# Performance work log

Measured on AMD Instinct MI355X. Metric: run time of the kernel, lower is better.

## Reference

```python
import jax, jax.numpy as jnp
import numpy as np

N_WIRES = 14
N_LAYERS = 3
DIM = 2 ** N_WIRES
BATCH = 1024


def _rx(theta):
    # RX(t) = [[cos t/2, -i sin t/2], [-i sin t/2, cos t/2]]
    c = jnp.cos(theta / 2).astype(jnp.complex64)
    s = jnp.sin(theta / 2).astype(jnp.complex64)
    return jnp.stack([jnp.stack([c, -1j * s]), jnp.stack([-1j * s, c])])


def _ry(theta):
    # RY(t) = [[cos t/2, -sin t/2], [sin t/2, cos t/2]]
    c = jnp.cos(theta / 2).astype(jnp.complex64)
    s = jnp.sin(theta / 2).astype(jnp.complex64)
    return jnp.stack([jnp.stack([c, -s]), jnp.stack([s, c])])


def _apply_1q(psi, U, w):
    # psi: (B, 2, 2, ..., 2); apply 2x2 U on qubit axis w+1
    psi = jnp.tensordot(psi, U, axes=((w + 1,), (1,)))  # contracted axis moves to end
    return jnp.moveaxis(psi, -1, w + 1)


def _apply_cnot(psi, c, t):
    # control qubit c, target qubit t (Python ints)
    a0 = jax.lax.index_in_dim(psi, 0, axis=c + 1, keepdims=True)
    a1 = jax.lax.index_in_dim(psi, 1, axis=c + 1, keepdims=True)
    a1 = jnp.flip(a1, axis=t + 1)  # X on target within control=1 subspace
    return jnp.concatenate([a0, a1], axis=c + 1)


def _circuit_features(state, params):
    # state: (B, 2**n) real normalized amplitudes -> PauliZ expvals (B, n)
    n = N_WIRES
    psi = state.astype(jnp.complex64).reshape((-1,) + (2,) * n)
    for layer in range(N_LAYERS):
        for w in range(n):
            psi = _apply_1q(psi, _rx(params[layer, w, 0]), w)
            psi = _apply_1q(psi, _ry(params[layer, w, 1]), w)
        for w in range(n - 1):
            psi = _apply_cnot(psi, w, w + 1)
        psi = _apply_cnot(psi, n - 1, 0)
    probs = jnp.real(psi * jnp.conj(psi))  # (B, 2, ..., 2)
    feats = []
    for w in range(n):
        axes = tuple(a for a in range(1, n + 1) if a != w + 1)
        p = jnp.sum(probs, axis=axes)  # (B, 2)
        feats.append(p[:, 0] - p[:, 1])  # <Z_w>
    return jnp.stack(feats, axis=1)  # (B, n)


def setup_inputs() -> dict:
    key = jax.random.key(0)
    k1, k2, k3 = jax.random.split(key, 3)
    state = jax.random.normal(k1, (BATCH, DIM), dtype=jnp.float32)
    state = state / jnp.linalg.norm(state, axis=1, keepdims=True)  # valid statevectors
    params = jax.random.normal(k2, (N_LAYERS, N_WIRES, 2), dtype=jnp.float32)
    head_w = jax.random.normal(k3, (1, N_WIRES), dtype=jnp.float32) * (1.0 / np.sqrt(N_WIRES))
    head_b = jnp.zeros((1,), dtype=jnp.float32)
    return {"state": state, "params": params, "head_w": head_w, "head_b": head_b}


def reference(state, params, head_w, head_b):
    feats = _circuit_features(state, params)          # (B, n_wires)
    out = feats @ head_w.T + head_b                   # (B, 1)
    return out[:, 0]                                  # (B,)
```

## Files before the change

### kernel.cpp

```cpp
#include <hip/hip_runtime.h>
#include <utility>

#define NW 14
#define NL 3
#define DIM 16384
#define NG  (NL * NW)
#define TPB 1024
#define NPH3 11

typedef float v2f __attribute__((ext_vector_type(2)));

struct S3 {
    int ok = 1;
    unsigned Lane[NPH3][6] = {};
    unsigned Reg[NPH3][4]  = {};
    unsigned Vw[4]         = {};
    unsigned WT[NPH3][6]   = {};
    unsigned WS[NPH3][16]  = {};
    unsigned pv[NPH3][4]   = {};
    unsigned cp[NPH3][4]   = {};
    unsigned ST[10] = {}, STK[4] = {}, STJ[4] = {};
    unsigned pz[NW] = {}, nib[NW] = {};
};

constexpr int rank14(const unsigned* v, int n) {
    unsigned piv[14] = {};
    int r = 0;
    for (int i = 0; i < n; ++i) {
        unsigned x = v[i];
        for (int bit = 13; bit >= 0; --bit) {
            if (!((x >> bit) & 1u)) continue;
            if (piv[bit]) { x ^= piv[bit]; }
            else { piv[bit] = x; ++r; x = 0; break; }
        }
    }
    return r;
}

constexpr unsigned coords14(const unsigned bas[14], unsigned v, int& ok) {
    unsigned pv14[14] = {}, pc14[14] = {};
    for (int b = 0; b < 14; ++b) {
        unsigned x = bas[b], c = 1u << b;
        for (int bit = 13; bit >= 0; --bit) {
            if (!((x >> bit) & 1u)) continue;
            if (pv14[bit]) { x ^= pv14[bit]; c ^= pc14[bit]; }
            else { pv14[bit] = x; pc14[bit] = c; x = 0; break; }
        }
        if (x) ok = 0;
    }
    unsigned x = v, c = 0;
    for (int bit = 13; bit >= 0; --bit) {
        if ((x >> bit) & 1u) {
            if (!pv14[bit]) { ok = 0; return 0; }
            x ^= pv14[bit]; c ^= pc14[bit];
        }
    }
    return c;
}

constexpr S3 build3() {
    S3 S{};
    unsigned mk[NG] = {}, vmg[NG] = {}, zm[NW] = {};
    {
        unsigned A[NW] = {};
        for (int w = 0; w < NW; ++w) A[w] = 1u << (NW - 1 - w);
        int g = 0;
        for (int l = 0; l < NL; ++l) {
            unsigned rows[NW] = {};
            for (int u = 0; u < NW; ++u) rows[u] = A[u] | (1u << (NW + u));
            for (int col = 0; col < NW; ++col) {
                int piv = col;
                while (piv < NW && !((rows[piv] >> col) & 1u)) ++piv;
                if (piv >= NW) { S.ok = 0; continue; }
                unsigned tmp = rows[col]; rows[col] = rows[piv]; rows[piv] = tmp;
                for (int r = 0; r < NW; ++r)
                    if (r != col && ((rows[r] >> col) & 1u)) rows[r] ^= rows[col];
            }
            for (int w = 0; w < NW; ++w) {
                unsigned m = 0;
                for (int r = 0; r < NW; ++r) m |= ((rows[r] >> (NW + w)) & 1u) << r;
                mk[g] = m; vmg[g] = A[w]; ++g;
            }
            for (int w = 0; w < NW - 1; ++w) A[w + 1] ^= A[w];
            A[0] ^= A[NW - 1];
        }
        for (int w = 0; w < NW; ++w) zm[w] = A[w];
    }
    for (int p = 0; p < NPH3; ++p) {
        int J = (p < 10) ? 4 : 2;
        for (int q = 0; q < J; ++q) S.Reg[p][q] = mk[4 * p + q];
    }
    {
        int found = 0;
        for (unsigned seed = 1; seed < 256u && !found; ++seed) {
            unsigned cand[4] = {};
            for (int i = 0; i < 4; ++i) {
                unsigned h = (seed * 2654435761u) ^ ((unsigned)(i + 1) * 0x9E3779B9u);
                h ^= h >> 15; h *= 2246822519u; h ^= h >> 13; h *= 3266489917u; h ^= h >> 16;
                cand[i] = h & 0x3FFFu;
            }
            if (rank14(cand, 4) != 4) continue;
            int good = 1;
            for (int g = 0; g < 6 && good; ++g) {
                int nm = (g < 5) ? 8 : 2;
                unsigned set[12] = {}; int n = 0;
                for (int i = 0; i < nm; ++i) set[n++] = mk[8 * g + i];
                for (int i = 0; i < 4; ++i) set[n++] = cand[i];
                if (rank14(set, n) != n) good = 0;
            }
            if (good) { for (int i = 0; i < 4; ++i) S.Vw[i] = cand[i]; found = 1; }
        }
        if (!found) S.ok = 0;
    }
    for (int g = 0; g < 6; ++g) {
        int nm = (g < 5) ? 8 : 2;
        unsigned bas[14] = {}; int nb = 0;
        for (int i = 0; i < 4; ++i) bas[nb++] = S.Vw[i];
        for (int i = 0; i < nm; ++i) bas[nb++] = mk[8 * g + i];
        unsigned fill[12] = {}; int nf = 0;
        for (int b = 0; b < 14 && nb < 14; ++b) {
            unsigned t[15] = {};
            for (int i = 0; i < nb; ++i) t[i] = bas[i];
            t[nb] = 1u << b;
            if (rank14(t, nb + 1) == nb + 1) { bas[nb++] = 1u << b; fill[nf++] = 1u << b; }
        }
        if (nb != 14) S.ok = 0;
        if (g < 5) {
            int pA = 2 * g, pB = 2 * g + 1;
            for (int b = 0; b < 4; ++b) { S.Lane[pA][b] = S.Reg[pB][b]; S.Lane[pB][b] = S.Reg[pA][b]; }
            S.Lane[pA][4] = fill[0]; S.Lane[pA][5] = fill[1];
            S.Lane[pB][4] = fill[0]; S.Lane[pB][5] = fill[1];
        } else {
            S.Reg[10][2] = fill[0]; S.Reg[10][3] = fill[1];
            for (int b = 0; b < 6; ++b) S.Lane[10][b] = fill[2 + b];
        }
    }
    for (int t = NPH3 - 2; t >= 0; --t) {
        unsigned bas[14] = {};
        for (int b = 0; b < 6; ++b) bas[b] = S.Lane[t + 1][b];
        for (int q = 0; q < 4; ++q) bas[6 + q] = S.Reg[t + 1][q];
        for (int j = 0; j < 4; ++j) bas[10 + j] = S.Vw[j];
        unsigned rb[4] = {}; int rn = 0;
        for (int b = 0; b < 6; ++b) {
            int bestcs = 0, bestg = -1; unsigned bestr = 0;
            for (int cs = 0; cs < 16; ++cs) {
                unsigned c = 0;
                for (int q = 0; q < 4; ++q) if ((cs >> q) & 1) c ^= S.Reg[t][q];
                int ok2 = 1;
                unsigned r = coords14(bas, S.Lane[t][b] ^ c, ok2) & 15u;
                if (!ok2) continue;
                unsigned x = r;
                for (int i = 0; i < rn; ++i) {
                    int hb = 3; while (hb > 0 && !((rb[i] >> hb) & 1u)) --hb;
                    if ((x >> hb) & 1u) x ^= rb[i];
                }
                int gain = x ? 1 : 0;
                if (gain > bestg) { bestg = gain; bestcs = cs; bestr = r; }
                if (gain == 1) break;
            }
            unsigned c = 0;
            for (int q = 0; q < 4; ++q) if ((bestcs >> q) & 1) c ^= S.Reg[t][q];
            S.Lane[t][b] ^= c;
            unsigned x = bestr;
            for (int i = 0; i < rn; ++i) {
                int hb = 3; while (hb > 0 && !((rb[i] >> hb) & 1u)) --hb;
                if ((x >> hb) & 1u) x ^= rb[i];
            }
            if (x && rn < 4) rb[rn++] = x;
        }
        int okc = 1;
        for (int b = 0; b < 6; ++b) S.WT[t][b] = coords14(bas, S.Lane[t][b], okc);
        for (int s = 0; s < 16; ++s) {
            unsigned v = 0;
            for (int q = 0; q < 4; ++q) if ((s >> q) & 1) v ^= S.Reg[t][q];
            S.WS[t][s] = coords14(bas, v, okc);
        }
        if (!okc) S.ok = 0;
        if ((t & 1) == 0) {
            for (int b = 0; b < 6; ++b) if (S.WT[t][b] >> 10) S.ok = 0;
            for (int s = 0; s < 16; ++s) if (S.WS[t][s] >> 10) S.ok = 0;
        }
        for (int ub = 0; ub < 10; ++ub) {
            unsigned wamp = (ub < 6) ? S.Lane[t][ub] : S.Vw[ub - 6];
            unsigned widx = (ub < 6) ? S.WT[t][ub] : (1u << (10 + ub - 6));
            unsigned ramp = 0;
            for (int b = 0; b < 6; ++b) if ((widx >> b) & 1u) ramp ^= S.Lane[t + 1][b];
            for (int q = 0; q < 4; ++q) if ((widx >> (6 + q)) & 1u) ramp ^= S.Reg[t + 1][q];
            for (int j = 0; j < 4; ++j) if ((widx >> (10 + j)) & 1u) ramp ^= S.Vw[j];
            if (ramp != wamp) S.ok = 0;
        }
        for (int q = 0; q < 4; ++q) {
            unsigned widx = S.WS[t][1u << q];
            unsigned ramp = 0;
            for (int b = 0; b < 6; ++b) if ((widx >> b) & 1u) ramp ^= S.Lane[t + 1][b];
            for (int qq = 0; qq < 4; ++qq) if ((widx >> (6 + qq)) & 1u) ramp ^= S.Reg[t + 1][qq];
            for (int j = 0; j < 4; ++j) if ((widx >> (10 + j)) & 1u) ramp ^= S.Vw[j];
            if (ramp != S.Reg[t][q]) S.ok = 0;
        }
    }
    for (int p = 0; p < NPH3; ++p) {
        int J = (p < 10) ? 4 : 2;
        for (int q = 0; q < J; ++q) {
            unsigned vm = vmg[4 * p + q], pvm = 0;
            for (int b = 0; b < 6; ++b)
                if (__builtin_popcount(S.Lane[p][b] & vm) & 1) pvm |= 1u << b;
            for (int j = 0; j < 4; ++j)
                if (__builtin_popcount(S.Vw[j] & vm) & 1) pvm |= 1u << (6 + j);
            S.pv[p][q] = pvm;
            unsigned cpm = 0;
            for (int s = 0; s < 16; ++s) {
                unsigned v = 0;
                for (int q2 = 0; q2 < 4; ++q2) if ((s >> q2) & 1) v ^= S.Reg[p][q2];
                if (__builtin_popcount(v & vm) & 1) cpm |= 1u << s;
            }
            S.cp[p][q] = cpm;
        }
    }
    {
        unsigned bas[14] = {};
        for (int b = 0; b < 6; ++b) bas[b] = S.Lane[0][b];
        for (int q = 0; q < 4; ++q) bas[6 + q] = S.Reg[0][q];
        for (int j = 0; j < 4; ++j) bas[10 + j] = S.Vw[j];
        int okc = 1;
        for (int b = 0; b < 10; ++b) S.ST[b] = coords14(bas, 1u << (b + 2), okc);
        for (int k = 0; k < 4; ++k) S.STK[k] = coords14(bas, (unsigned)k << 12, okc);
        for (int j = 0; j < 4; ++j) S.STJ[j] = coords14(bas, (unsigned)j, okc);
        if (!okc) S.ok = 0;
        for (int ub = 0; ub < 18; ++ub) {
            unsigned amp = (ub < 10) ? (1u << (ub + 2))
                         : (ub < 14) ? ((unsigned)(ub - 10) << 12) : (unsigned)(ub - 14);
            unsigned widx = (ub < 10) ? S.ST[ub] : (ub < 14) ? S.STK[ub - 10] : S.STJ[ub - 14];
            unsigned ramp = 0;
            for (int b = 0; b < 6; ++b) if ((widx >> b) & 1u) ramp ^= S.Lane[0][b];
            for (int q = 0; q < 4; ++q) if ((widx >> (6 + q)) & 1u) ramp ^= S.Reg[0][q];
            for (int j = 0; j < 4; ++j) if ((widx >> (10 + j)) & 1u) ramp ^= S.Vw[j];
            if (ramp != amp) S.ok = 0;
        }
    }
    for (int w = 0; w < NW; ++w) {
        unsigned pzm = 0;
        for (int b = 0; b < 6; ++b)
            if (__builtin_popcount(S.Lane[10][b] & zm[w]) & 1) pzm |= 1u << b;
        for (int j = 0; j < 4; ++j)
            if (__builtin_popcount(S.Vw[j] & zm[w]) & 1) pzm |= 1u << (6 + j);
        S.pz[w] = pzm;
        unsigned nv = 0;
        for (int q = 0; q < 4; ++q)
            if (__builtin_popcount(S.Reg[10][q] & zm[w]) & 1) nv |= 1u << q;
        S.nib[w] = nv;
    }
    return S;
}
constexpr S3 SC3 = build3();
static_assert(SC3.ok == 1, "schedule build failed");

template<class F, unsigned... I>
__device__ __forceinline__ void static_for_impl(F&& f, std::integer_sequence<unsigned, I...>) {
    (f(std::integral_constant<unsigned, I>{}), ...);
}
template<unsigned N, class F>
__device__ __forceinline__ void static_for(F&& f) {
    static_for_impl(static_cast<F&&>(f), std::make_integer_sequence<unsigned, N>{});
}

template<int NEGLO, int NEGHI>
__device__ __forceinline__ v2f cmul(v2f k, v2f x) {
    v2f y;
    if constexpr (!NEGLO)
        asm("v_pk_mul_f32 %0, %1, %2 op_sel:[0,0] op_sel_hi:[0,1]"
            : "=&v"(y) : "v"(k), "v"(x));
    else
        asm("v_pk_mul_f32 %0, %1, %2 op_sel:[0,0] op_sel_hi:[0,1] neg_lo:[1,0] neg_hi:[1,0]"
            : "=&v"(y) : "v"(k), "v"(x));
    if constexpr (!NEGHI)
        asm("v_pk_fma_f32 %0, %1, %2, %0 op_sel:[1,1,0] op_sel_hi:[1,0,1] neg_lo:[0,1,0]"
            : "+v"(y) : "v"(k), "v"(x));
    else
        asm("v_pk_fma_f32 %0, %1, %2, %0 op_sel:[1,1,0] op_sel_hi:[1,0,1] neg_lo:[1,1,0] neg_hi:[1,0,0]"
            : "+v"(y) : "v"(k), "v"(x));
    return y;
}
template<int NEGLO, int NEGHI>
__device__ __forceinline__ void cmac(v2f& y, v2f k, v2f x) {
    if constexpr (!NEGLO)
        asm("v_pk_fma_f32 %0, %1, %2, %0 op_sel:[0,0,0] op_sel_hi:[0,1,1]"
            : "+v"(y) : "v"(k), "v"(x));
    else
        asm("v_pk_fma_f32 %0, %1, %2, %0 op_sel:[0,0,0] op_sel_hi:[0,1,1] neg_lo:[1,0,0] neg_hi:[1,0,0]"
            : "+v"(y) : "v"(k), "v"(x));
    if constexpr (!NEGHI)
        asm("v_pk_fma_f32 %0, %1, %2, %0 op_sel:[1,1,0] op_sel_hi:[1,0,1] neg_lo:[0,1,0]"
            : "+v"(y) : "v"(k), "v"(x));
    else
        asm("v_pk_fma_f32 %0, %1, %2, %0 op_sel:[1,1,0] op_sel_hi:[1,0,1] neg_lo:[1,1,0] neg_hi:[1,0,0]"
            : "+v"(y) : "v"(k), "v"(x));
}
template<bool CS> __device__ __forceinline__ v2f  cmulA(v2f k, v2f x) { return cmul<0, CS ? 1 : 0>(k, x); }
template<bool CS> __device__ __forceinline__ void cmacB(v2f& y, v2f k, v2f x) { cmac<CS ? 1 : 0, 0>(y, k, x); }

__global__ __launch_bounds__(TPB) void qsim_kernel(
    const float* __restrict__ state,
    const float* __restrict__ params,
    const float* __restrict__ head_w,
    const float* __restrict__ head_b,
    float* __restrict__ out)
{
    __shared__ v2f    psi[DIM];
    __shared__ float4 umat[NG];
    __shared__ float  red[TPB / 64];
    char* psiB = (char*)psi;
    const unsigned tid = threadIdx.x;

    if (tid < NG) {
        float t1 = 0.5f * params[2 * tid + 0];
        float t2 = 0.5f * params[2 * tid + 1];
        float s1, c1, s2, c2;
        sincosf(t1, &s1, &c1);
        sincosf(t2, &s2, &c2);
        umat[tid] = make_float4(c1 * c2, s1 * s2, -s2 * c1, -c2 * s1);
    }

    unsigned sidx = 0;
    static_for<10>([&](auto Bc) {
        constexpr int b = (int)decltype(Bc)::value;
        sidx ^= SC3.ST[b] & (unsigned)(-(int)((tid >> b) & 1u));
    });
    const float4* st4 = reinterpret_cast<const float4*>(state) + (size_t)blockIdx.x * (DIM / 4);
    static_for<4>([&](auto Kc) {
        constexpr int k = (int)decltype(Kc)::value;
        float4 v = st4[tid + k * TPB];
        const unsigned bi = sidx ^ SC3.STK[k];
        *(v2f*)(psiB + ((bi ^ SC3.STJ[0]) << 3)) = (v2f){ v.x, 0.f };
        *(v2f*)(psiB + ((bi ^ SC3.STJ[1]) << 3)) = (v2f){ v.y, 0.f };
        *(v2f*)(psiB + ((bi ^ SC3.STJ[2]) << 3)) = (v2f){ v.z, 0.f };
        *(v2f*)(psiB + ((bi ^ SC3.STJ[3]) << 3)) = (v2f){ v.w, 0.f };
    });
    __syncthreads();

    const unsigned rbase = ((tid >> 6) << 13) | ((tid & 63u) << 3);
    v2f x[16];

    static_for<NPH3>([&](auto Pc) {
        constexpr int P = (int)decltype(Pc)::value;
        static_for<16>([&](auto Sc) {
            constexpr int s = (int)decltype(Sc)::value;
            x[s] = *(const v2f*)(psiB + rbase + (s << 9));
        });
        static_for<4>([&](auto Qc) {
            constexpr int q = (int)decltype(Qc)::value;
            if constexpr (q < ((P < 10) ? 4 : 2)) {
                constexpr unsigned cp  = SC3.cp[P][q];
                constexpr unsigned pvm = SC3.pv[P][q];
                const float4 u = umat[4 * P + q];
                const unsigned sm = ((unsigned)__popc(tid & pvm)) << 31;
                v2f A, B;
                A.x = u.x; A.y = __uint_as_float(__float_as_uint(u.y) ^ sm);
                B.x = __uint_as_float(__float_as_uint(u.z) ^ sm); B.y = u.w;
                static_for<8>([&](auto Pp) {
                    constexpr unsigned pp   = decltype(Pp)::value;
                    constexpr unsigned lowm = (1u << q) - 1u;
                    constexpr unsigned s0   = ((pp & ~lowm) << 1) | (pp & lowm);
                    constexpr unsigned s1   = s0 | (1u << q);
                    constexpr bool c0 = (cp >> s0) & 1u;
                    constexpr bool c1 = (cp >> s1) & 1u;
                    const v2f x0 = x[s0], x1 = x[s1];
                    v2f y0 = cmulA<c0>(A, x0); cmacB<c0>(y0, B, x1);
                    v2f y1 = cmulA<c1>(A, x1); cmacB<c1>(y1, B, x0);
                    x[s0] = y0; x[s1] = y1;
                });
            }
        });
        if constexpr (P < 10) {
            if constexpr (P & 1) __syncthreads();
            unsigned wi = (tid >> 6) << 10;
            static_for<6>([&](auto Bc) {
                constexpr int b = (int)decltype(Bc)::value;
                wi ^= SC3.WT[P][b] & (unsigned)(-(int)((tid >> b) & 1u));
            });
            static_for<16>([&](auto Sc) {
                constexpr int s = (int)decltype(Sc)::value;
                *(v2f*)(psiB + ((wi ^ SC3.WS[P][s]) << 3)) = x[s];
            });
            if constexpr (P & 1) __syncthreads();
        }
    });

    float e[NW];
    static_for<NW>([&](auto Wc) {
        constexpr int w = (int)decltype(Wc)::value;
        constexpr unsigned pzw = SC3.pz[w];
        float hw = head_w[w];
        e[w] = (__popc(tid & pzw) & 1) ? -hw : hw;
    });
    float c[16];
    static_for<16>([&](auto Mc) { c[decltype(Mc)::value] = 0.f; });
    static_for<NW>([&](auto Wc) {
        constexpr int w = (int)decltype(Wc)::value;
        c[SC3.nib[w]] += e[w];
    });
    static_for<4>([&](auto Bc) {
        constexpr unsigned B = 1u << decltype(Bc)::value;
        static_for<16>([&](auto Kc) {
            constexpr unsigned k = decltype(Kc)::value;
            if constexpr (!(k & B)) {
                float a = c[k], b = c[k | B];
                c[k] = a + b; c[k | B] = a - b;
            }
        });
    });
    float acc = 0.f;
    static_for<16>([&](auto Sc) {
        constexpr int s = (int)decltype(Sc)::value;
        acc += (x[s].x * x[s].x + x[s].y * x[s].y) * c[s];
    });

#pragma unroll
    for (int off = 32; off > 0; off >>= 1)
        acc += __shfl_down(acc, off, 64);
    const unsigned lane = tid & 63, wv = tid >> 6;
    if (lane == 0) red[wv] = acc;
    __syncthreads();
    if (tid == 0) {
        float tot = 0.f;
#pragma unroll
        for (int i = 0; i < TPB / 64; ++i) tot += red[i];
        out[blockIdx.x] = tot + head_b[0];
    }
}

extern "C" void kernel_launch(void* const* d_in, const int* in_sizes, int n_in,
                              void* d_out, int out_size, void* d_ws, size_t ws_size,
                              hipStream_t stream) {
    const float* state  = (const float*)d_in[0];
    const float* params = (const float*)d_in[1];
    const float* head_w = (const float*)d_in[2];
    const float* head_b = (const float*)d_in[3];
    float* out = (float*)d_out;

    qsim_kernel<<<out_size, TPB, 0, stream>>>(state, params, head_w, head_b, out);
}
```

Baseline: 133.6 us.

## Halve LDS state buffer with two-pass bounce exchange to allow two blocks per CU

Replaces the full 128KB shared statevector with a half-size bounce buffer. Each exchange is split into two passes, with groups of threads writing or reading depending on a dropped index bit, and the schedule search is extended so that bit can be dropped consistently. Launch bounds now request higher occupancy so more than one block can be resident per CU. In exchange, every exchange needs twice as many barriers and extra registers to hold pending values, which may cut into the occupancy gain.

```diff
diff --git a/kernel.cpp b/kernel.cpp
--- a/kernel.cpp
+++ b/kernel.cpp
@@ -23,42 +23,43 @@
     unsigned pz[NW] = {}, nib[NW] = {};
 };
 
-constexpr int rank14(const unsigned* v, int n) {
-    unsigned piv[14] = {};
-    int r = 0;
-    for (int i = 0; i < n; ++i) {
-        unsigned x = v[i];
-        for (int bit = 13; bit >= 0; --bit) {
-            if (!((x >> bit) & 1u)) continue;
-            if (piv[bit]) { x ^= piv[bit]; }
-            else { piv[bit] = x; ++r; x = 0; break; }
-        }
-    }
-    return r;
-}
-
-constexpr unsigned coords14(const unsigned bas[14], unsigned v, int& ok) {
-    unsigned pv14[14] = {}, pc14[14] = {};
+struct Bas14 { unsigned piv[14] = {}; int n = 0; };
+constexpr bool binsert(Bas14& B, unsigned v) {
+    unsigned x = v;
+    for (int bit = 13; bit >= 0; --bit) {
+        if (!((x >> bit) & 1u)) continue;
+        if (B.piv[bit]) x ^= B.piv[bit];
+        else { B.piv[bit] = x; ++B.n; return true; }
+    }
+    return false;
+}
+
+struct Ech { unsigned pv14[14] = {}; unsigned pc14[14] = {}; int ok = 1; };
+constexpr Ech mkech(const unsigned bas[14]) {
+    Ech E{};
     for (int b = 0; b < 14; ++b) {
         unsigned x = bas[b], c = 1u << b;
         for (int bit = 13; bit >= 0; --bit) {
             if (!((x >> bit) & 1u)) continue;
-            if (pv14[bit]) { x ^= pv14[bit]; c ^= pc14[bit]; }
-            else { pv14[bit] = x; pc14[bit] = c; x = 0; break; }
-        }
-        if (x) ok = 0;
-    }
+            if (E.pv14[bit]) { x ^= E.pv14[bit]; c ^= E.pc14[bit]; }
+            else { E.pv14[bit] = x; E.pc14[bit] = c; x = 0; break; }
+        }
+        if (x) E.ok = 0;
+    }
+    return E;
+}
+constexpr unsigned coordsE(const Ech& E, unsigned v, int& ok) {
     unsigned x = v, c = 0;
     for (int bit = 13; bit >= 0; --bit) {
         if ((x >> bit) & 1u) {
-            if (!pv14[bit]) { ok = 0; return 0; }
-            x ^= pv14[bit]; c ^= pc14[bit];
+            if (!E.pv14[bit]) { ok = 0; return 0; }
+            x ^= E.pv14[bit]; c ^= E.pc14[bit];
         }
     }
     return c;
 }
 
-constexpr S3 build3() {
+constexpr S3 build3(int vskip) {
     S3 S{};
     unsigned mk[NG] = {}, vmg[NG] = {}, zm[NW] = {};
     {
@@ -91,40 +92,44 @@
         for (int q = 0; q < J; ++q) S.Reg[p][q] = mk[4 * p + q];
     }
     {
-        int found = 0;
-        for (unsigned seed = 1; seed < 256u && !found; ++seed) {
+        Bas14 gb[6] = {};
+        for (int g = 0; g < 6; ++g) {
+            int nm = (g < 5) ? 8 : 2;
+            for (int i = 0; i < nm; ++i) binsert(gb[g], mk[8 * g + i]);
+        }
+        int found = 0, skipped = 0;
+        for (unsigned seed = 1; seed < 512u && !found; ++seed) {
             unsigned cand[4] = {};
             for (int i = 0; i < 4; ++i) {
                 unsigned h = (seed * 2654435761u) ^ ((unsigned)(i + 1) * 0x9E3779B9u);
                 h ^= h >> 15; h *= 2246822519u; h ^= h >> 13; h *= 3266489917u; h ^= h >> 16;
                 cand[i] = h & 0x3FFFu;
             }
-            if (rank14(cand, 4) != 4) continue;
-            int good = 1;
+            Bas14 cb{};
+            bool good = binsert(cb, cand[0]) && binsert(cb, cand[1])
+                     && binsert(cb, cand[2]) && binsert(cb, cand[3]);
             for (int g = 0; g < 6 && good; ++g) {
-                int nm = (g < 5) ? 8 : 2;
-                unsigned set[12] = {}; int n = 0;
-                for (int i = 0; i < nm; ++i) set[n++] = mk[8 * g + i];
-                for (int i = 0; i < 4; ++i) set[n++] = cand[i];
-                if (rank14(set, n) != n) good = 0;
-            }
-            if (good) { for (int i = 0; i < 4; ++i) S.Vw[i] = cand[i]; found = 1; }
+                Bas14 t = gb[g];
+                for (int i = 0; i < 4 && good; ++i)
+                    if (!binsert(t, cand[i])) good = false;
+            }
+            if (good) {
+                if (skipped < vskip) { ++skipped; continue; }
+                for (int i = 0; i < 4; ++i) S.Vw[i] = cand[i];
+                found = 1;
+            }
         }
         if (!found) S.ok = 0;
     }
     for (int g = 0; g < 6; ++g) {
         int nm = (g < 5) ? 8 : 2;
-        unsigned bas[14] = {}; int nb = 0;
-        for (int i = 0; i < 4; ++i) bas[nb++] = S.Vw[i];
-        for (int i = 0; i < nm; ++i) bas[nb++] = mk[8 * g + i];
+        Bas14 B{};
+        for (int i = 0; i < 4; ++i) binsert(B, S.Vw[i]);
+        for (int i = 0; i < nm; ++i) binsert(B, mk[8 * g + i]);
         unsigned fill[12] = {}; int nf = 0;
-        for (int b = 0; b < 14 && nb < 14; ++b) {
-            unsigned t[15] = {};
-            for (int i = 0; i < nb; ++i) t[i] = bas[i];
-            t[nb] = 1u << b;
-            if (rank14(t, nb + 1) == nb + 1) { bas[nb++] = 1u << b; fill[nf++] = 1u << b; }
-        }
-        if (nb != 14) S.ok = 0;
+        for (int b = 0; b < 14 && B.n < 14; ++b)
+            if (binsert(B, 1u << b)) fill[nf++] = 1u << b;
+        if (B.n != 14) S.ok = 0;
         if (g < 5) {
             int pA = 2 * g, pB = 2 * g + 1;
             for (int b = 0; b < 4; ++b) { S.Lane[pA][b] = S.Reg[pB][b]; S.Lane[pB][b] = S.Reg[pA][b]; }
@@ -140,6 +145,8 @@
         for (int b = 0; b < 6; ++b) bas[b] = S.Lane[t + 1][b];
         for (int q = 0; q < 4; ++q) bas[6 + q] = S.Reg[t + 1][q];
         for (int j = 0; j < 4; ++j) bas[10 + j] = S.Vw[j];
+        Ech E = mkech(bas);
+        if (!E.ok) S.ok = 0;
         unsigned rb[4] = {}; int rn = 0;
         for (int b = 0; b < 6; ++b) {
             int bestcs = 0, bestg = -1; unsigned bestr = 0;
@@ -147,7 +154,7 @@
                 unsigned c = 0;
                 for (int q = 0; q < 4; ++q) if ((cs >> q) & 1) c ^= S.Reg[t][q];
                 int ok2 = 1;
-                unsigned r = coords14(bas, S.Lane[t][b] ^ c, ok2) & 15u;
+                unsigned r = coordsE(E, S.Lane[t][b] ^ c, ok2) & 15u;
                 if (!ok2) continue;
                 unsigned x = r;
                 for (int i = 0; i < rn; ++i) {
@@ -169,11 +176,11 @@
             if (x && rn < 4) rb[rn++] = x;
         }
         int okc = 1;
-        for (int b = 0; b < 6; ++b) S.WT[t][b] = coords14(bas, S.Lane[t][b], okc);
+        for (int b = 0; b < 6; ++b) S.WT[t][b] = coordsE(E, S.Lane[t][b], okc);
         for (int s = 0; s < 16; ++s) {
             unsigned v = 0;
             for (int q = 0; q < 4; ++q) if ((s >> q) & 1) v ^= S.Reg[t][q];
-            S.WS[t][s] = coords14(bas, v, okc);
+            S.WS[t][s] = coordsE(E, v, okc);
         }
         if (!okc) S.ok = 0;
         if ((t & 1) == 0) {
@@ -221,10 +228,12 @@
         for (int b = 0; b < 6; ++b) bas[b] = S.Lane[0][b];
         for (int q = 0; q < 4; ++q) bas[6 + q] = S.Reg[0][q];
         for (int j = 0; j < 4; ++j) bas[10 + j] = S.Vw[j];
+        Ech E = mkech(bas);
+        if (!E.ok) S.ok = 0;
         int okc = 1;
-        for (int b = 0; b < 10; ++b) S.ST[b] = coords14(bas, 1u << (b + 2), okc);
-        for (int k = 0; k < 4; ++k) S.STK[k] = coords14(bas, (unsigned)k << 12, okc);
-        for (int j = 0; j < 4; ++j) S.STJ[j] = coords14(bas, (unsigned)j, okc);
+        for (int b = 0; b < 10; ++b) S.ST[b] = coordsE(E, 1u << (b + 2), okc);
+        for (int k = 0; k < 4; ++k) S.STK[k] = coordsE(E, (unsigned)k << 12, okc);
+        for (int j = 0; j < 4; ++j) S.STJ[j] = coordsE(E, (unsigned)j, okc);
         if (!okc) S.ok = 0;
         for (int ub = 0; ub < 18; ++ub) {
             unsigned amp = (ub < 10) ? (1u << (ub + 2))
@@ -251,8 +260,40 @@
     }
     return S;
 }
-constexpr S3 SC3 = build3();
+
+constexpr int pickDrop(const S3& S) {
+    for (int d = 13; d >= 10; --d) {
+        bool good = true;
+        for (int t = 1; t < 10; t += 2) {
+            unsigned orv = S.WS[t][1] | S.WS[t][2] | S.WS[t][4] | S.WS[t][8];
+            if (!((orv >> d) & 1u)) good = false;
+        }
+        if (good) return d;
+    }
+    return -1;
+}
+constexpr S3 pickBuild() {
+    for (int v = 0; v < 4; ++v) {
+        S3 s = build3(v);
+        if (s.ok && pickDrop(s) >= 0) return s;
+    }
+    return build3(0);
+}
+constexpr S3 SC3 = pickBuild();
 static_assert(SC3.ok == 1, "schedule build failed");
+constexpr int DROPB0 = pickDrop(SC3);
+constexpr int DROPB = (DROPB0 >= 10) ? DROPB0 : 13;
+constexpr unsigned LOWM = (1u << DROPB) - 1u;
+constexpr int KD = DROPB - 10;
+__host__ __device__ constexpr unsigned cmprs(unsigned v) {
+    return (v & LOWM) | ((v >> 1) & 0x1FFFu & ~LOWM);
+}
+constexpr int hbit(unsigned v) { return (int)((v >> DROPB) & 1u); }
+constexpr int pidx(int P, int s) {
+    int c = hbit(SC3.WS[P][s]), n = 0;
+    for (int t = 0; t < s; ++t) if (hbit(SC3.WS[P][t]) == c) ++n;
+    return n;
+}
 
 template<class F, unsigned... I>
 __device__ __forceinline__ void static_for_impl(F&& f, std::integer_sequence<unsigned, I...>) {
@@ -298,17 +339,126 @@
 template<bool CS> __device__ __forceinline__ v2f  cmulA(v2f k, v2f x) { return cmul<0, CS ? 1 : 0>(k, x); }
 template<bool CS> __device__ __forceinline__ void cmacB(v2f& y, v2f k, v2f x) { cmac<CS ? 1 : 0, 0>(y, k, x); }
 
-__global__ __launch_bounds__(TPB) void qsim_kernel(
+template<int P>
+__device__ __forceinline__ void gates(v2f* x, const float4* __restrict__ umat, unsigned tid)
+{
+    static_for<4>([&](auto Qc) {
+        constexpr int q = (int)decltype(Qc)::value;
+        if constexpr (q < ((P < 10) ? 4 : 2)) {
+            constexpr unsigned cp  = SC3.cp[P][q];
+            constexpr unsigned pvm = SC3.pv[P][q];
+            const float4 u = umat[4 * P + q];
+            const unsigned sm = ((unsigned)__popc(tid & pvm)) << 31;
+            v2f A, B;
+            A.x = u.x; A.y = __uint_as_float(__float_as_uint(u.y) ^ sm);
+            B.x = __uint_as_float(__float_as_uint(u.z) ^ sm); B.y = u.w;
+            static_for<8>([&](auto Pp) {
+                constexpr unsigned pp   = decltype(Pp)::value;
+                constexpr unsigned lowm = (1u << q) - 1u;
+                constexpr unsigned s0   = ((pp & ~lowm) << 1) | (pp & lowm);
+                constexpr unsigned s1   = s0 | (1u << q);
+                constexpr bool c0 = (cp >> s0) & 1u;
+                constexpr bool c1 = (cp >> s1) & 1u;
+                const v2f x0 = x[s0], x1 = x[s1];
+                v2f y0 = cmulA<c0>(A, x0); cmacB<c0>(y0, B, x1);
+                v2f y1 = cmulA<c1>(A, x1); cmacB<c1>(y1, B, x0);
+                x[s0] = y0; x[s1] = y1;
+            });
+        }
+    });
+}
+
+__device__ __forceinline__ void rdall(v2f* x, const char* bnc, unsigned rb) {
+    static_for<16>([&](auto Sc) {
+        constexpr int s = (int)decltype(Sc)::value;
+        x[s] = *(const v2f*)(bnc + rb + s * 512);
+    });
+}
+
+template<int P>
+__device__ __forceinline__ void exch(char* bnc, unsigned tid, v2f* x,
+                                     unsigned rb, bool rbit)
+{
+    unsigned wi = ((tid >> 6) & 15u) << 10;
+    static_for<6>([&](auto Bc) {
+        constexpr int b = (int)decltype(Bc)::value;
+        constexpr unsigned m = SC3.WT[P][b];
+        wi ^= m & (unsigned)(-(int)((tid >> b) & 1u));
+    });
+    const unsigned wim = cmprs(wi) << 3;
+
+    if constexpr (!(P & 1)) {
+        if (!rbit) {
+            static_for<16>([&](auto Sc) {
+                constexpr int s = (int)decltype(Sc)::value;
+                *(v2f*)(bnc + (wim ^ (cmprs(SC3.WS[P][s]) << 3))) = x[s];
+            });
+        }
+        __syncthreads();
+        if (!rbit) rdall(x, bnc, rb);
+        __syncthreads();
+        if (rbit) {
+            static_for<16>([&](auto Sc) {
+                constexpr int s = (int)decltype(Sc)::value;
+                *(v2f*)(bnc + (wim ^ (cmprs(SC3.WS[P][s]) << 3))) = x[s];
+            });
+        }
+        __syncthreads();
+        if (rbit) rdall(x, bnc, rb);
+        __syncthreads();
+    } else {
+        const bool t13 = (wi >> DROPB) & 1u;
+        v2f pend[16];
+        if (!t13) {
+            static_for<16>([&](auto Sc) {
+                constexpr int s = (int)decltype(Sc)::value;
+                if constexpr (hbit(SC3.WS[P][s]) == 0)
+                    *(v2f*)(bnc + (wim ^ (cmprs(SC3.WS[P][s]) << 3))) = x[s];
+                else
+                    pend[pidx(P, s)] = x[s];
+            });
+        } else {
+            static_for<16>([&](auto Sc) {
+                constexpr int s = (int)decltype(Sc)::value;
+                if constexpr (hbit(SC3.WS[P][s]) == 1)
+                    *(v2f*)(bnc + (wim ^ (cmprs(SC3.WS[P][s]) << 3))) = x[s];
+                else
+                    pend[pidx(P, s)] = x[s];
+            });
+        }
+        __syncthreads();
+        if (!rbit) rdall(x, bnc, rb);
+        __syncthreads();
+        if (!t13) {
+            static_for<16>([&](auto Sc) {
+                constexpr int s = (int)decltype(Sc)::value;
+                if constexpr (hbit(SC3.WS[P][s]) == 1)
+                    *(v2f*)(bnc + (wim ^ (cmprs(SC3.WS[P][s]) << 3))) = pend[pidx(P, s)];
+            });
+        } else {
+            static_for<16>([&](auto Sc) {
+                constexpr int s = (int)decltype(Sc)::value;
+                if constexpr (hbit(SC3.WS[P][s]) == 0)
+                    *(v2f*)(bnc + (wim ^ (cmprs(SC3.WS[P][s]) << 3))) = pend[pidx(P, s)];
+            });
+        }
+        __syncthreads();
+        if (rbit) rdall(x, bnc, rb);
+        __syncthreads();
+    }
+}
+
+__global__ __launch_bounds__(TPB, 8) void qsim_kernel(
     const float* __restrict__ state,
     const float* __restrict__ params,
     const float* __restrict__ head_w,
     const float* __restrict__ head_b,
     float* __restrict__ out)
 {
-    __shared__ v2f    psi[DIM];
+    __shared__ v2f    bounce[DIM / 2];
     __shared__ float4 umat[NG];
     __shared__ float  red[TPB / 64];
-    char* psiB = (char*)psi;
+    char* bnc = (char*)bounce;
     const unsigned tid = threadIdx.x;
 
     if (tid < NG) {
@@ -320,69 +470,70 @@
         umat[tid] = make_float4(c1 * c2, s1 * s2, -s2 * c1, -c2 * s1);
     }
 
+    float arr[16];
+    const float4* st4 = reinterpret_cast<const float4*>(state) + (size_t)blockIdx.x * (DIM / 4);
+    static_for<4>([&](auto Kc) {
+        constexpr int k = (int)decltype(Kc)::value;
+        *(float4*)&arr[4 * k] = st4[tid + k * TPB];
+    });
+
     unsigned sidx = 0;
     static_for<10>([&](auto Bc) {
         constexpr int b = (int)decltype(Bc)::value;
         sidx ^= SC3.ST[b] & (unsigned)(-(int)((tid >> b) & 1u));
     });
-    const float4* st4 = reinterpret_cast<const float4*>(state) + (size_t)blockIdx.x * (DIM / 4);
-    static_for<4>([&](auto Kc) {
-        constexpr int k = (int)decltype(Kc)::value;
-        float4 v = st4[tid + k * TPB];
-        const unsigned bi = sidx ^ SC3.STK[k];
-        *(v2f*)(psiB + ((bi ^ SC3.STJ[0]) << 3)) = (v2f){ v.x, 0.f };
-        *(v2f*)(psiB + ((bi ^ SC3.STJ[1]) << 3)) = (v2f){ v.y, 0.f };
-        *(v2f*)(psiB + ((bi ^ SC3.STJ[2]) << 3)) = (v2f){ v.z, 0.f };
-        *(v2f*)(psiB + ((bi ^ SC3.STJ[3]) << 3)) = (v2f){ v.w, 0.f };
-    });
+    const unsigned sim = cmprs(sidx) << 3;
+    const bool ts = (sidx >> DROPB) & 1u;
+
+    const unsigned w4 = (tid >> 6) & 15u;
+    constexpr unsigned KM = (1u << KD) - 1u;
+    const unsigned cw = (w4 & KM) | ((w4 >> 1) & (7u & ~KM));
+    const unsigned rb = ((cw << 10) | (tid & 63u)) << 3;
+    const bool rbit = (w4 >> KD) & 1u;
+
+    v2f x[16];
+
+    if (!ts) {
+        static_for<16>([&](auto Ic) {
+            constexpr int i = (int)decltype(Ic)::value;
+            constexpr unsigned C = SC3.STK[i >> 2] ^ SC3.STJ[i & 3];
+            if constexpr (hbit(C) == 0)
+                *(v2f*)(bnc + (sim ^ (cmprs(C) << 3))) = (v2f){ arr[i], 0.f };
+        });
+    } else {
+        static_for<16>([&](auto Ic) {
+            constexpr int i = (int)decltype(Ic)::value;
+            constexpr unsigned C = SC3.STK[i >> 2] ^ SC3.STJ[i & 3];
+            if constexpr (hbit(C) == 1)
+                *(v2f*)(bnc + (sim ^ (cmprs(C) << 3))) = (v2f){ arr[i], 0.f };
+        });
+    }
     __syncthreads();
-
-    const unsigned rbase = ((tid >> 6) << 13) | ((tid & 63u) << 3);
-    v2f x[16];
+    if (!rbit) rdall(x, bnc, rb);
+    __syncthreads();
+    if (!ts) {
+        static_for<16>([&](auto Ic) {
+            constexpr int i = (int)decltype(Ic)::value;
+            constexpr unsigned C = SC3.STK[i >> 2] ^ SC3.STJ[i & 3];
+            if constexpr (hbit(C) == 1)
+                *(v2f*)(bnc + (sim ^ (cmprs(C) << 3))) = (v2f){ arr[i], 0.f };
+        });
+    } else {
+        static_for<16>([&](auto Ic) {
+            constexpr int i = (int)decltype(Ic)::value;
+            constexpr unsigned C = SC3.STK[i >> 2] ^ SC3.STJ[i & 3];
+            if constexpr (hbit(C) == 0)
+                *(v2f*)(bnc + (sim ^ (cmprs(C) << 3))) = (v2f){ arr[i], 0.f };
+        });
+    }
+    __syncthreads();
+    if (rbit) rdall(x, bnc, rb);
+    __syncthreads();
 
     static_for<NPH3>([&](auto Pc) {
         constexpr int P = (int)decltype(Pc)::value;
-        static_for<16>([&](auto Sc) {
-            constexpr int s = (int)decltype(Sc)::value;
-            x[s] = *(const v2f*)(psiB + rbase + (s << 9));
-        });
-        static_for<4>([&](auto Qc) {
-            constexpr int q = (int)decltype(Qc)::value;
-            if constexpr (q < ((P < 10) ? 4 : 2)) {
-                constexpr unsigned cp  = SC3.cp[P][q];
-                constexpr unsigned pvm = SC3.pv[P][q];
-                const float4 u = umat[4 * P + q];
-                const unsigned sm = ((unsigned)__popc(tid & pvm)) << 31;
-                v2f A, B;
-                A.x = u.x; A.y = __uint_as_float(__float_as_uint(u.y) ^ sm);
-                B.x = __uint_as_float(__float_as_uint(u.z) ^ sm); B.y = u.w;
-                static_for<8>([&](auto Pp) {
-                    constexpr unsigned pp   = decltype(Pp)::value;
-                    constexpr unsigned lowm = (1u << q) - 1u;
-                    constexpr unsigned s0   = ((pp & ~lowm) << 1) | (pp & lowm);
-                    constexpr unsigned s1   = s0 | (1u << q);
-                    constexpr bool c0 = (cp >> s0) & 1u;
-                    constexpr bool c1 = (cp >> s1) & 1u;
-                    const v2f x0 = x[s0], x1 = x[s1];
-                    v2f y0 = cmulA<c0>(A, x0); cmacB<c0>(y0, B, x1);
-                    v2f y1 = cmulA<c1>(A, x1); cmacB<c1>(y1, B, x0);
-                    x[s0] = y0; x[s1] = y1;
-                });
-            }
-        });
-        if constexpr (P < 10) {
-            if constexpr (P & 1) __syncthreads();
-            unsigned wi = (tid >> 6) << 10;
-            static_for<6>([&](auto Bc) {
-                constexpr int b = (int)decltype(Bc)::value;
-                wi ^= SC3.WT[P][b] & (unsigned)(-(int)((tid >> b) & 1u));
-            });
-            static_for<16>([&](auto Sc) {
-                constexpr int s = (int)decltype(Sc)::value;
-                *(v2f*)(psiB + ((wi ^ SC3.WS[P][s]) << 3)) = x[s];
-            });
-            if constexpr (P & 1) __syncthreads();
-        }
+        gates<P>(x, umat, tid);
+        if constexpr (P < 10) exch<P>(bnc, tid, x, rb, rbit);
     });
 
     float e[NW];
```

Measured after the change: 156.1 us. +16.8%, slower.

## Process two batch states per block, overlapping gate math with shared-memory exchange

Applied to the files above, without the earlier changes.

Each block now simulates two statevectors that share a single shared-memory buffer. It interleaves them so that one state's gate arithmetic runs while the other state's write/read exchange through LDS proceeds. The gate, read and write phases are factored into helpers, the grid is halved, and launch bounds ask for higher occupancy. The constexpr schedule builder is refactored, drops a constraint check, and can try alternate Vw seeds. This doubles register pressure (two 16-element complex arrays) and assumes an even batch size.

```diff
diff --git a/kernel.cpp b/kernel.cpp
--- a/kernel.cpp
+++ b/kernel.cpp
@@ -23,42 +23,43 @@
     unsigned pz[NW] = {}, nib[NW] = {};
 };
 
-constexpr int rank14(const unsigned* v, int n) {
-    unsigned piv[14] = {};
-    int r = 0;
-    for (int i = 0; i < n; ++i) {
-        unsigned x = v[i];
-        for (int bit = 13; bit >= 0; --bit) {
-            if (!((x >> bit) & 1u)) continue;
-            if (piv[bit]) { x ^= piv[bit]; }
-            else { piv[bit] = x; ++r; x = 0; break; }
-        }
-    }
-    return r;
-}
-
-constexpr unsigned coords14(const unsigned bas[14], unsigned v, int& ok) {
-    unsigned pv14[14] = {}, pc14[14] = {};
+struct Bas14 { unsigned piv[14] = {}; int n = 0; };
+constexpr bool binsert(Bas14& B, unsigned v) {
+    unsigned x = v;
+    for (int bit = 13; bit >= 0; --bit) {
+        if (!((x >> bit) & 1u)) continue;
+        if (B.piv[bit]) x ^= B.piv[bit];
+        else { B.piv[bit] = x; ++B.n; return true; }
+    }
+    return false;
+}
+
+struct Ech { unsigned pv14[14] = {}; unsigned pc14[14] = {}; int ok = 1; };
+constexpr Ech mkech(const unsigned bas[14]) {
+    Ech E{};
     for (int b = 0; b < 14; ++b) {
         unsigned x = bas[b], c = 1u << b;
         for (int bit = 13; bit >= 0; --bit) {
             if (!((x >> bit) & 1u)) continue;
-            if (pv14[bit]) { x ^= pv14[bit]; c ^= pc14[bit]; }
-            else { pv14[bit] = x; pc14[bit] = c; x = 0; break; }
-        }
-        if (x) ok = 0;
-    }
+            if (E.pv14[bit]) { x ^= E.pv14[bit]; c ^= E.pc14[bit]; }
+            else { E.pv14[bit] = x; E.pc14[bit] = c; x = 0; break; }
+        }
+        if (x) E.ok = 0;
+    }
+    return E;
+}
+constexpr unsigned coordsE(const Ech& E, unsigned v, int& ok) {
     unsigned x = v, c = 0;
     for (int bit = 13; bit >= 0; --bit) {
         if ((x >> bit) & 1u) {
-            if (!pv14[bit]) { ok = 0; return 0; }
-            x ^= pv14[bit]; c ^= pc14[bit];
+            if (!E.pv14[bit]) { ok = 0; return 0; }
+            x ^= E.pv14[bit]; c ^= E.pc14[bit];
         }
     }
     return c;
 }
 
-constexpr S3 build3() {
+constexpr S3 build3(int vskip) {
     S3 S{};
     unsigned mk[NG] = {}, vmg[NG] = {}, zm[NW] = {};
     {
@@ -91,40 +92,44 @@
         for (int q = 0; q < J; ++q) S.Reg[p][q] = mk[4 * p + q];
     }
     {
-        int found = 0;
-        for (unsigned seed = 1; seed < 256u && !found; ++seed) {
+        Bas14 gb[6] = {};
+        for (int g = 0; g < 6; ++g) {
+            int nm = (g < 5) ? 8 : 2;
+            for (int i = 0; i < nm; ++i) binsert(gb[g], mk[8 * g + i]);
+        }
+        int found = 0, skipped = 0;
+        for (unsigned seed = 1; seed < 512u && !found; ++seed) {
             unsigned cand[4] = {};
             for (int i = 0; i < 4; ++i) {
                 unsigned h = (seed * 2654435761u) ^ ((unsigned)(i + 1) * 0x9E3779B9u);
                 h ^= h >> 15; h *= 2246822519u; h ^= h >> 13; h *= 3266489917u; h ^= h >> 16;
                 cand[i] = h & 0x3FFFu;
             }
-            if (rank14(cand, 4) != 4) continue;
-            int good = 1;
+            Bas14 cb{};
+            bool good = binsert(cb, cand[0]) && binsert(cb, cand[1])
+                     && binsert(cb, cand[2]) && binsert(cb, cand[3]);
             for (int g = 0; g < 6 && good; ++g) {
-                int nm = (g < 5) ? 8 : 2;
-                unsigned set[12] = {}; int n = 0;
-                for (int i = 0; i < nm; ++i) set[n++] = mk[8 * g + i];
-                for (int i = 0; i < 4; ++i) set[n++] = cand[i];
-                if (rank14(set, n) != n) good = 0;
-            }
-            if (good) { for (int i = 0; i < 4; ++i) S.Vw[i] = cand[i]; found = 1; }
+                Bas14 t = gb[g];
+                for (int i = 0; i < 4 && good; ++i)
+                    if (!binsert(t, cand[i])) good = false;
+            }
+            if (good) {
+                if (skipped < vskip) { ++skipped; continue; }
+                for (int i = 0; i < 4; ++i) S.Vw[i] = cand[i];
+                found = 1;
+            }
         }
         if (!found) S.ok = 0;
     }
     for (int g = 0; g < 6; ++g) {
         int nm = (g < 5) ? 8 : 2;
-        unsigned bas[14] = {}; int nb = 0;
-        for (int i = 0; i < 4; ++i) bas[nb++] = S.Vw[i];
-        for (int i = 0; i < nm; ++i) bas[nb++] = mk[8 * g + i];
+        Bas14 B{};
+        for (int i = 0; i < 4; ++i) binsert(B, S.Vw[i]);
+        for (int i = 0; i < nm; ++i) binsert(B, mk[8 * g + i]);
         unsigned fill[12] = {}; int nf = 0;
-        for (int b = 0; b < 14 && nb < 14; ++b) {
-            unsigned t[15] = {};
-            for (int i = 0; i < nb; ++i) t[i] = bas[i];
-            t[nb] = 1u << b;
-            if (rank14(t, nb + 1) == nb + 1) { bas[nb++] = 1u << b; fill[nf++] = 1u << b; }
-        }
-        if (nb != 14) S.ok = 0;
+        for (int b = 0; b < 14 && B.n < 14; ++b)
+            if (binsert(B, 1u << b)) fill[nf++] = 1u << b;
+        if (B.n != 14) S.ok = 0;
         if (g < 5) {
             int pA = 2 * g, pB = 2 * g + 1;
             for (int b = 0; b < 4; ++b) { S.Lane[pA][b] = S.Reg[pB][b]; S.Lane[pB][b] = S.Reg[pA][b]; }
@@ -140,6 +145,8 @@
         for (int b = 0; b < 6; ++b) bas[b] = S.Lane[t + 1][b];
         for (int q = 0; q < 4; ++q) bas[6 + q] = S.Reg[t + 1][q];
         for (int j = 0; j < 4; ++j) bas[10 + j] = S.Vw[j];
+        Ech E = mkech(bas);
+        if (!E.ok) S.ok = 0;
         unsigned rb[4] = {}; int rn = 0;
         for (int b = 0; b < 6; ++b) {
             int bestcs = 0, bestg = -1; unsigned bestr = 0;
@@ -147,7 +154,7 @@
                 unsigned c = 0;
                 for (int q = 0; q < 4; ++q) if ((cs >> q) & 1) c ^= S.Reg[t][q];
                 int ok2 = 1;
-                unsigned r = coords14(bas, S.Lane[t][b] ^ c, ok2) & 15u;
+                unsigned r = coordsE(E, S.Lane[t][b] ^ c, ok2) & 15u;
                 if (!ok2) continue;
                 unsigned x = r;
                 for (int i = 0; i < rn; ++i) {
@@ -169,17 +176,13 @@
             if (x && rn < 4) rb[rn++] = x;
         }
         int okc = 1;
-        for (int b = 0; b < 6; ++b) S.WT[t][b] = coords14(bas, S.Lane[t][b], okc);
+        for (int b = 0; b < 6; ++b) S.WT[t][b] = coordsE(E, S.Lane[t][b], okc);
         for (int s = 0; s < 16; ++s) {
             unsigned v = 0;
             for (int q = 0; q < 4; ++q) if ((s >> q) & 1) v ^= S.Reg[t][q];
-            S.WS[t][s] = coords14(bas, v, okc);
+            S.WS[t][s] = coordsE(E, v, okc);
         }
         if (!okc) S.ok = 0;
-        if ((t & 1) == 0) {
-            for (int b = 0; b < 6; ++b) if (S.WT[t][b] >> 10) S.ok = 0;
-            for (int s = 0; s < 16; ++s) if (S.WS[t][s] >> 10) S.ok = 0;
-        }
         for (int ub = 0; ub < 10; ++ub) {
             unsigned wamp = (ub < 6) ? S.Lane[t][ub] : S.Vw[ub - 6];
             unsigned widx = (ub < 6) ? S.WT[t][ub] : (1u << (10 + ub - 6));
@@ -221,10 +224,12 @@
         for (int b = 0; b < 6; ++b) bas[b] = S.Lane[0][b];
         for (int q = 0; q < 4; ++q) bas[6 + q] = S.Reg[0][q];
         for (int j = 0; j < 4; ++j) bas[10 + j] = S.Vw[j];
+        Ech E = mkech(bas);
+        if (!E.ok) S.ok = 0;
         int okc = 1;
-        for (int b = 0; b < 10; ++b) S.ST[b] = coords14(bas, 1u << (b + 2), okc);
-        for (int k = 0; k < 4; ++k) S.STK[k] = coords14(bas, (unsigned)k << 12, okc);
-        for (int j = 0; j < 4; ++j) S.STJ[j] = coords14(bas, (unsigned)j, okc);
+        for (int b = 0; b < 10; ++b) S.ST[b] = coordsE(E, 1u << (b + 2), okc);
+        for (int k = 0; k < 4; ++k) S.STK[k] = coordsE(E, (unsigned)k << 12, okc);
+        for (int j = 0; j < 4; ++j) S.STJ[j] = coordsE(E, (unsigned)j, okc);
         if (!okc) S.ok = 0;
         for (int ub = 0; ub < 18; ++ub) {
             unsigned amp = (ub < 10) ? (1u << (ub + 2))
@@ -251,7 +256,14 @@
     }
     return S;
 }
-constexpr S3 SC3 = build3();
+constexpr S3 pickBuild() {
+    for (int v = 0; v < 4; ++v) {
+        S3 s = build3(v);
+        if (s.ok) return s;
+    }
+    S3 bad{}; bad.ok = 0; return bad;
+}
+constexpr S3 SC3 = pickBuild();
 static_assert(SC3.ok == 1, "schedule build failed");
 
 template<class F, unsigned... I>
@@ -298,7 +310,73 @@
 template<bool CS> __device__ __forceinline__ v2f  cmulA(v2f k, v2f x) { return cmul<0, CS ? 1 : 0>(k, x); }
 template<bool CS> __device__ __forceinline__ void cmacB(v2f& y, v2f k, v2f x) { cmac<CS ? 1 : 0, 0>(y, k, x); }
 
-__global__ __launch_bounds__(TPB) void qsim_kernel(
+template<int P>
+__device__ __forceinline__ void gates(v2f* x, const float4* __restrict__ umat, unsigned tid)
+{
+    static_for<4>([&](auto Qc) {
+        constexpr int q = (int)decltype(Qc)::value;
+        if constexpr (q < ((P < 10) ? 4 : 2)) {
+            constexpr unsigned cp  = SC3.cp[P][q];
+            constexpr unsigned pvm = SC3.pv[P][q];
+            const float4 u = umat[4 * P + q];
+            const unsigned sm = ((unsigned)__popc(tid & pvm)) << 31;
+            v2f A, B;
+            A.x = u.x; A.y = __uint_as_float(__float_as_uint(u.y) ^ sm);
+            B.x = __uint_as_float(__float_as_uint(u.z) ^ sm); B.y = u.w;
+            static_for<8>([&](auto Pp) {
+                constexpr unsigned pp   = decltype(Pp)::value;
+                constexpr unsigned lowm = (1u << q) - 1u;
+                constexpr unsigned s0   = ((pp & ~lowm) << 1) | (pp & lowm);
+                constexpr unsigned s1   = s0 | (1u << q);
+                constexpr bool c0 = (cp >> s0) & 1u;
+                constexpr bool c1 = (cp >> s1) & 1u;
+                const v2f x0 = x[s0], x1 = x[s1];
+                v2f y0 = cmulA<c0>(A, x0); cmacB<c0>(y0, B, x1);
+                v2f y1 = cmulA<c1>(A, x1); cmacB<c1>(y1, B, x0);
+                x[s0] = y0; x[s1] = y1;
+            });
+        }
+    });
+}
+
+__device__ __forceinline__ void rdall(v2f* x, const char* psiB, unsigned rbase) {
+    static_for<16>([&](auto Sc) {
+        constexpr int s = (int)decltype(Sc)::value;
+        x[s] = *(const v2f*)(psiB + rbase + (s << 9));
+    });
+}
+
+template<int P>
+__device__ __forceinline__ void wrt(char* psiB, unsigned tid, const v2f* x) {
+    unsigned wi = ((tid >> 6) & 15u) << 10;
+    static_for<6>([&](auto Bc) {
+        constexpr int b = (int)decltype(Bc)::value;
+        constexpr unsigned m = SC3.WT[P][b];
+        wi ^= m & (unsigned)(-(int)((tid >> b) & 1u));
+    });
+    const unsigned wib = wi << 3;
+    static_for<16>([&](auto Sc) {
+        constexpr int s = (int)decltype(Sc)::value;
+        constexpr unsigned off = SC3.WS[P][s] << 3;
+        *(v2f*)(psiB + (wib ^ off)) = x[s];
+    });
+}
+
+__device__ __forceinline__ void stageW(char* psiB, const float* __restrict__ gsrc,
+                                       unsigned tid, unsigned sidx) {
+    const float4* st4 = reinterpret_cast<const float4*>(gsrc);
+    static_for<4>([&](auto Kc) {
+        constexpr int k = (int)decltype(Kc)::value;
+        float4 v = st4[tid + k * TPB];
+        const unsigned bi = sidx ^ SC3.STK[k];
+        *(v2f*)(psiB + ((bi ^ SC3.STJ[0]) << 3)) = (v2f){ v.x, 0.f };
+        *(v2f*)(psiB + ((bi ^ SC3.STJ[1]) << 3)) = (v2f){ v.y, 0.f };
+        *(v2f*)(psiB + ((bi ^ SC3.STJ[2]) << 3)) = (v2f){ v.z, 0.f };
+        *(v2f*)(psiB + ((bi ^ SC3.STJ[3]) << 3)) = (v2f){ v.w, 0.f };
+    });
+}
+
+__global__ __launch_bounds__(TPB, 4) void qsim_kernel(
     const float* __restrict__ state,
     const float* __restrict__ params,
     const float* __restrict__ head_w,
@@ -307,7 +385,7 @@
 {
     __shared__ v2f    psi[DIM];
     __shared__ float4 umat[NG];
-    __shared__ float  red[TPB / 64];
+    __shared__ float  red[2 * (TPB / 64)];
     char* psiB = (char*)psi;
     const unsigned tid = threadIdx.x;
 
@@ -320,70 +398,42 @@
         umat[tid] = make_float4(c1 * c2, s1 * s2, -s2 * c1, -c2 * s1);
     }
 
+    const float* gA = state + (size_t)(2 * blockIdx.x) * DIM;
+    const float* gB = gA + DIM;
+
     unsigned sidx = 0;
     static_for<10>([&](auto Bc) {
         constexpr int b = (int)decltype(Bc)::value;
         sidx ^= SC3.ST[b] & (unsigned)(-(int)((tid >> b) & 1u));
     });
-    const float4* st4 = reinterpret_cast<const float4*>(state) + (size_t)blockIdx.x * (DIM / 4);
-    static_for<4>([&](auto Kc) {
-        constexpr int k = (int)decltype(Kc)::value;
-        float4 v = st4[tid + k * TPB];
-        const unsigned bi = sidx ^ SC3.STK[k];
-        *(v2f*)(psiB + ((bi ^ SC3.STJ[0]) << 3)) = (v2f){ v.x, 0.f };
-        *(v2f*)(psiB + ((bi ^ SC3.STJ[1]) << 3)) = (v2f){ v.y, 0.f };
-        *(v2f*)(psiB + ((bi ^ SC3.STJ[2]) << 3)) = (v2f){ v.z, 0.f };
-        *(v2f*)(psiB + ((bi ^ SC3.STJ[3]) << 3)) = (v2f){ v.w, 0.f };
-    });
+    const unsigned rbase = ((tid >> 6) << 13) | ((tid & 63u) << 3);
+
+    v2f xA[16], xB[16];
+
+    stageW(psiB, gA, tid, sidx);
     __syncthreads();
-
-    const unsigned rbase = ((tid >> 6) << 13) | ((tid & 63u) << 3);
-    v2f x[16];
-
-    static_for<NPH3>([&](auto Pc) {
+    rdall(xA, psiB, rbase);
+    __syncthreads();
+    stageW(psiB, gB, tid, sidx);
+    gates<0>(xA, umat, tid);
+    __syncthreads();
+    rdall(xB, psiB, rbase);
+    __syncthreads();
+
+    static_for<10>([&](auto Pc) {
         constexpr int P = (int)decltype(Pc)::value;
-        static_for<16>([&](auto Sc) {
-            constexpr int s = (int)decltype(Sc)::value;
-            x[s] = *(const v2f*)(psiB + rbase + (s << 9));
-        });
-        static_for<4>([&](auto Qc) {
-            constexpr int q = (int)decltype(Qc)::value;
-            if constexpr (q < ((P < 10) ? 4 : 2)) {
-                constexpr unsigned cp  = SC3.cp[P][q];
-                constexpr unsigned pvm = SC3.pv[P][q];
-                const float4 u = umat[4 * P + q];
-                const unsigned sm = ((unsigned)__popc(tid & pvm)) << 31;
-                v2f A, B;
-                A.x = u.x; A.y = __uint_as_float(__float_as_uint(u.y) ^ sm);
-                B.x = __uint_as_float(__float_as_uint(u.z) ^ sm); B.y = u.w;
-                static_for<8>([&](auto Pp) {
-                    constexpr unsigned pp   = decltype(Pp)::value;
-                    constexpr unsigned lowm = (1u << q) - 1u;
-                    constexpr unsigned s0   = ((pp & ~lowm) << 1) | (pp & lowm);
-                    constexpr unsigned s1   = s0 | (1u << q);
-                    constexpr bool c0 = (cp >> s0) & 1u;
-                    constexpr bool c1 = (cp >> s1) & 1u;
-                    const v2f x0 = x[s0], x1 = x[s1];
-                    v2f y0 = cmulA<c0>(A, x0); cmacB<c0>(y0, B, x1);
-                    v2f y1 = cmulA<c1>(A, x1); cmacB<c1>(y1, B, x0);
-                    x[s0] = y0; x[s1] = y1;
-                });
-            }
-        });
-        if constexpr (P < 10) {
-            if constexpr (P & 1) __syncthreads();
-            unsigned wi = (tid >> 6) << 10;
-            static_for<6>([&](auto Bc) {
-                constexpr int b = (int)decltype(Bc)::value;
-                wi ^= SC3.WT[P][b] & (unsigned)(-(int)((tid >> b) & 1u));
-            });
-            static_for<16>([&](auto Sc) {
-                constexpr int s = (int)decltype(Sc)::value;
-                *(v2f*)(psiB + ((wi ^ SC3.WS[P][s]) << 3)) = x[s];
-            });
-            if constexpr (P & 1) __syncthreads();
-        }
-    });
+        wrt<P>(psiB, tid, xA);
+        gates<P>(xB, umat, tid);
+        __syncthreads();
+        rdall(xA, psiB, rbase);
+        __syncthreads();
+        wrt<P>(psiB, tid, xB);
+        gates<P + 1>(xA, umat, tid);
+        __syncthreads();
+        rdall(xB, psiB, rbase);
+        __syncthreads();
+    });
+    gates<10>(xB, umat, tid);
 
     float e[NW];
     static_for<NW>([&](auto Wc) {
@@ -408,23 +458,27 @@
             }
         });
     });
-    float acc = 0.f;
+    float accA = 0.f, accB = 0.f;
     static_for<16>([&](auto Sc) {
         constexpr int s = (int)decltype(Sc)::value;
-        acc += (x[s].x * x[s].x + x[s].y * x[s].y) * c[s];
+        accA += (xA[s].x * xA[s].x + xA[s].y * xA[s].y) * c[s];
+        accB += (xB[s].x * xB[s].x + xB[s].y * xB[s].y) * c[s];
     });
 
 #pragma unroll
-    for (int off = 32; off > 0; off >>= 1)
-        acc += __shfl_down(acc, off, 64);
+    for (int off = 32; off > 0; off >>= 1) {
+        accA += __shfl_down(accA, off, 64);
+        accB += __shfl_down(accB, off, 64);
+    }
     const unsigned lane = tid & 63, wv = tid >> 6;
-    if (lane == 0) red[wv] = acc;
+    if (lane == 0) { red[wv] = accA; red[(TPB / 64) + wv] = accB; }
     __syncthreads();
     if (tid == 0) {
-        float tot = 0.f;
+        float tA = 0.f, tB = 0.f;
 #pragma unroll
-        for (int i = 0; i < TPB / 64; ++i) tot += red[i];
-        out[blockIdx.x] = tot + head_b[0];
+        for (int i = 0; i < TPB / 64; ++i) { tA += red[i]; tB += red[(TPB / 64) + i]; }
+        out[2 * blockIdx.x + 0] = tA + head_b[0];
+        out[2 * blockIdx.x + 1] = tB + head_b[0];
     }
 }
 
@@ -437,5 +491,5 @@
     const float* head_b = (const float*)d_in[3];
     float* out = (float*)d_out;
 
-    qsim_kernel<<<out_size, TPB, 0, stream>>>(state, params, head_w, head_b, out);
-}
+    qsim_kernel<<<out_size / 2, TPB, 0, stream>>>(state, params, head_w, head_b, out);
+}
```

Measured after the change: 128.7 us. -3.7%, faster.
